# Performance work log

Hardware: AMD Instinct MI355X
Metric: run time of the kernel (lower is better)

Reference implementation:

```python
import jax, jax.numpy as jnp
import numpy as np

HEADS = 12


def setup_inputs() -> dict:
    rng = jax.random.key(0)
    ks = jax.random.split(rng, 12)
    B, L, D = 8, 64, 768
    s = 1.0 / np.sqrt(D)  # keep projections well-scaled
    return {
        "key": jax.random.normal(ks[0], (B, L, L, D), jnp.float32),
        "value": jax.random.normal(ks[1], (B, L, L, D), jnp.float32),
        "query": jax.random.normal(ks[2], (B, L, D), jnp.float32),
        "mask": jnp.ones((B, L, L), jnp.float32),
        "Wk": jax.random.normal(ks[3], (D, D), jnp.float32) * s,
        "bk": jax.random.normal(ks[4], (D,), jnp.float32) * 0.01,
        "Wv": jax.random.normal(ks[5], (D, D), jnp.float32) * s,
        "bv": jax.random.normal(ks[6], (D,), jnp.float32) * 0.01,
        "Wq": jax.random.normal(ks[7], (D, D), jnp.float32) * s,
        "bq": jax.random.normal(ks[8], (D,), jnp.float32) * 0.01,
        "Wo": jax.random.normal(ks[9], (D, D), jnp.float32) * s,
        "bo": jax.random.normal(ks[10], (D,), jnp.float32) * 0.01,
    }


def reference(key, value, query, mask, Wk, bk, Wv, bv, Wq, bq, Wo, bo):
    # key/value: [B, L, L, D]; query: [B, L, D]; mask: [B, L, L]
    B, L, _, D = key.shape
    h = HEADS
    d = D // h
    # Projections (torch Linear y = x W^T + b; here W stored transposed so y = x @ W + b)
    Kp = (key @ Wk + bk).reshape(B, L, L, h, d)    # [B, i, j, h, d]
    Vp = (value @ Wv + bv).reshape(B, L, L, h, d)  # [B, i, j, h, d]
    Qp = (query @ Wq + bq).reshape(B, L, h, d)     # [B, i, h, d]
    Qp = Qp / jnp.sqrt(jnp.asarray(d, Qp.dtype))
    # scores[b,h,i,j] = sum_d Q[b,i,h,d] * K[b,i,j,h,d]  (query i attends over its own j-row)
    scores = jnp.einsum('bihd,bijhd->bhij', Qp, Kp)
    # multiplicative mask (as in the original: scores = scores * mask)
    scores = scores * mask[:, None, :, :]
    attn = jax.nn.softmax(scores, axis=-1)
    # dropout is identity at inference
    ctx = jnp.einsum('bhij,bijhd->bihd', attn, Vp).reshape(B, L, D)
    return ctx @ Wo + bo  # [B, L, D]
```

## Files before the change

### kernel.cpp

```cpp
#include <hip/hip_runtime.h>

#define DMODEL 768
#define NHEADS 12
#define RTOT   512
#define BIW    9216

__global__ __launch_bounds__(256) void linear16(
    const float* __restrict__ src, int ars, int scm,
    const float* __restrict__ W, const float* __restrict__ bias,
    float* __restrict__ dst, int drs, float scale)
{
    __shared__ float At[16][64];
    __shared__ float Bt[64][32];
    const int rt = blockIdx.x, ct = blockIdx.y, t = threadIdx.x;
    const int sk = ((ct * 32) >> 6) * scm;
    const int c  = t & 31;
    const int rg = t >> 5;

    const int ar0 = t >> 4,          ak0 = t & 15;
    const int bk0 = t >> 3,          bc0 = (t & 7) * 4;
    const int bk1 = (t + 256) >> 3,  bc1 = ((t + 256) & 7) * 4;

    float4 va0, vb0, vb1;
    auto LD = [&](int kb) {
        va0 = *(const float4*)&src[(size_t)(rt * 16 + ar0) * ars + sk + kb * 64 + ak0 * 4];
        vb0 = *(const float4*)&W[(size_t)(kb * 64 + bk0) * DMODEL + ct * 32 + bc0];
        vb1 = *(const float4*)&W[(size_t)(kb * 64 + bk1) * DMODEL + ct * 32 + bc1];
    };

    LD(0);
    float acc[2] = {0.f, 0.f};

    for (int kb = 0; kb < 12; ++kb) {
        if (kb) __syncthreads();
        *(float4*)&At[ar0][ak0 * 4] = va0;
        *(float4*)&Bt[bk0][bc0] = vb0;
        *(float4*)&Bt[bk1][bc1] = vb1;
        __syncthreads();
        if (kb < 11) LD(kb + 1);
        #pragma unroll
        for (int kq = 0; kq < 16; ++kq) {
            float b0 = Bt[kq * 4 + 0][c], b1 = Bt[kq * 4 + 1][c];
            float b2 = Bt[kq * 4 + 2][c], b3 = Bt[kq * 4 + 3][c];
            #pragma unroll
            for (int i = 0; i < 2; ++i) {
                float4 a = *(const float4*)&At[rg * 2 + i][kq * 4];
                acc[i] += a.x * b0 + a.y * b1 + a.z * b2 + a.w * b3;
            }
        }
    }
    const float bb = bias[ct * 32 + c];
    #pragma unroll
    for (int i = 0; i < 2; ++i)
        dst[(size_t)(rt * 16 + rg * 2 + i) * drs + ct * 32 + c] = (acc[i] + bb) * scale;
}

__global__ __launch_bounds__(256) void u_kernel(
    const float* __restrict__ qp, const float* __restrict__ Wk, const float* __restrict__ bk,
    float* __restrict__ u, float* __restrict__ cvec)
{
    __shared__ float Qt[32][64];
    __shared__ float Bt[64][65];
    const int rt = blockIdx.x, mt = blockIdx.y, h = blockIdx.z, t = threadIdx.x;

    #pragma unroll
    for (int kk = 0; kk < 2; ++kk) {
        int i4 = t + kk * 256;
        int r = i4 >> 4, dq = i4 & 15;
        *(float4*)&Qt[r][dq * 4] =
            *(const float4*)&qp[(size_t)(rt * 32 + r) * DMODEL + h * 64 + dq * 4];
    }
    #pragma unroll
    for (int kk = 0; kk < 4; ++kk) {
        int i4 = t + kk * 256;
        int m = i4 >> 4, dq = i4 & 15;
        float4 v = *(const float4*)&Wk[(size_t)(mt * 64 + m) * DMODEL + h * 64 + dq * 4];
        Bt[m][dq * 4 + 0] = v.x; Bt[m][dq * 4 + 1] = v.y;
        Bt[m][dq * 4 + 2] = v.z; Bt[m][dq * 4 + 3] = v.w;
    }
    __syncthreads();

    const int c = t & 63, rg = t >> 6;
    float acc[8] = {0.f,0.f,0.f,0.f,0.f,0.f,0.f,0.f};
    #pragma unroll
    for (int dq = 0; dq < 16; ++dq) {
        float b0 = Bt[c][dq * 4 + 0], b1 = Bt[c][dq * 4 + 1];
        float b2 = Bt[c][dq * 4 + 2], b3 = Bt[c][dq * 4 + 3];
        #pragma unroll
        for (int i = 0; i < 8; ++i) {
            float4 a = *(const float4*)&Qt[rg * 8 + i][dq * 4];
            acc[i] += a.x * b0 + a.y * b1 + a.z * b2 + a.w * b3;
        }
    }
    #pragma unroll
    for (int i = 0; i < 8; ++i)
        u[(size_t)(rt * 32 + rg * 8 + i) * BIW + h * DMODEL + mt * 64 + c] = acc[i];

    if (mt == 0 && t < 32) {
        float s = 0.f;
        for (int d = 0; d < 64; ++d) s += bk[h * 64 + d] * Qt[t][d];
        cvec[(rt * 32 + t) * NHEADS + h] = s;
    }
}

__global__ __launch_bounds__(256) void scores_k(
    const float* __restrict__ key, const float* __restrict__ u,
    const float* __restrict__ cvec, const float* __restrict__ mask,
    float* __restrict__ sc_out)
{
    const int bi   = blockIdx.x;
    const int jh   = blockIdx.y;
    const int t    = threadIdx.x;
    const int lane = t & 63;
    const int wv   = t >> 6;
    const size_t kvb = (size_t)bi * 64 * DMODEL;
    const float* ub = u + (size_t)bi * BIW + lane * 4;

    #pragma unroll
    for (int pass = 0; pass < 4; ++pass) {
        const int j0 = jh * 32 + wv * 8 + pass * 2;
        float a[NHEADS][2];
        #pragma unroll
        for (int h = 0; h < NHEADS; ++h) { a[h][0] = 0.f; a[h][1] = 0.f; }

        const float* k0 = &key[kvb + (size_t)j0 * DMODEL + lane * 4];
        float4 kc[2], kn[2];
        kc[0] = *(const float4*)k0;
        kc[1] = *(const float4*)(k0 + DMODEL);

        #pragma unroll
        for (int cch = 0; cch < 3; ++cch) {
            if (cch < 2) {
                kn[0] = *(const float4*)(k0 + (cch + 1) * 256);
                kn[1] = *(const float4*)(k0 + DMODEL + (cch + 1) * 256);
            }
            #pragma unroll
            for (int h = 0; h < NHEADS; ++h) {
                float4 u4 = *(const float4*)(ub + h * DMODEL + cch * 256);
                a[h][0] += kc[0].x * u4.x + kc[0].y * u4.y + kc[0].z * u4.z + kc[0].w * u4.w;
                a[h][1] += kc[1].x * u4.x + kc[1].y * u4.y + kc[1].z * u4.z + kc[1].w * u4.w;
            }
            kc[0] = kn[0];
            kc[1] = kn[1];
        }

        #pragma unroll
        for (int r = 0; r < 2; ++r) {
            float s6[6];
            #pragma unroll
            for (int i = 0; i < 6; ++i) {
                float lo = a[i][r], hi = a[i + 6][r];
                float tl = __shfl_xor(lo, 32), th = __shfl_xor(hi, 32);
                s6[i] = (lane < 32) ? lo + tl : hi + th;
            }
            float s3[3];
            #pragma unroll
            for (int i = 0; i < 3; ++i) {
                float lo = s6[i], hi = s6[i + 3];
                float tl = __shfl_xor(lo, 16), th = __shfl_xor(hi, 16);
                s3[i] = ((lane & 16) == 0) ? lo + tl : hi + th;
            }
            #pragma unroll
            for (int o = 8; o >= 1; o >>= 1)
                #pragma unroll
                for (int i = 0; i < 3; ++i) s3[i] += __shfl_xor(s3[i], o);
            if ((lane & 15) == 0) {
                const int g = lane >> 4;
                const int j = j0 + r;
                const float mk = mask[bi * 64 + j];
                #pragma unroll
                for (int i = 0; i < 3; ++i) {
                    const int h = g * 3 + i;
                    sc_out[(size_t)bi * 768 + h * 64 + j] =
                        (s3[i] + cvec[bi * NHEADS + h]) * mk;
                }
            }
        }
    }
}

__global__ __launch_bounds__(256) void pv_k(
    const float* __restrict__ value, const float* __restrict__ sc,
    float* __restrict__ w)
{
    __shared__ float attn[NHEADS][64];

    const int bi   = blockIdx.x;
    const int ms   = blockIdx.y;
    const int t    = threadIdx.x;
    const int lane = t & 63;
    const int wv   = t >> 6;
    const size_t kvb = (size_t)bi * 64 * DMODEL;

    #pragma unroll
    for (int i = 0; i < 3; ++i) {
        const int h = wv * 3 + i;
        float s = sc[(size_t)bi * 768 + h * 64 + lane];
        float mx = s;
        #pragma unroll
        for (int o = 1; o < 64; o <<= 1) mx = fmaxf(mx, __shfl_xor(mx, o));
        float e = __expf(s - mx);
        float sm = e;
        #pragma unroll
        for (int o = 1; o < 64; o <<= 1) sm += __shfl_xor(sm, o);
        attn[h][lane] = e / sm;
    }
    __syncthreads();

    const int mo = ms * 256 + t;
    float acc[NHEADS];
    #pragma unroll
    for (int h = 0; h < NHEADS; ++h) acc[h] = 0.f;
    const float* vb = value + kvb + mo;

    #pragma unroll 2
    for (int j4 = 0; j4 < 64; j4 += 4) {
        float v0 = vb[(size_t)(j4 + 0) * DMODEL];
        float v1 = vb[(size_t)(j4 + 1) * DMODEL];
        float v2 = vb[(size_t)(j4 + 2) * DMODEL];
        float v3 = vb[(size_t)(j4 + 3) * DMODEL];
        #pragma unroll
        for (int h = 0; h < NHEADS; ++h) {
            float4 at = *(const float4*)&attn[h][j4];
            acc[h] += at.x * v0 + at.y * v1 + at.z * v2 + at.w * v3;
        }
    }
    #pragma unroll
    for (int h = 0; h < NHEADS; ++h)
        w[(size_t)bi * BIW + h * DMODEL + mo] = acc[h];
}

extern "C" void kernel_launch(void* const* d_in, const int* in_sizes, int n_in,
                              void* d_out, int out_size, void* d_ws, size_t ws_size,
                              hipStream_t stream) {
    const float* key   = (const float*)d_in[0];
    const float* value = (const float*)d_in[1];
    const float* query = (const float*)d_in[2];
    const float* mask  = (const float*)d_in[3];
    const float* Wk    = (const float*)d_in[4];
    const float* bk    = (const float*)d_in[5];
    const float* Wv    = (const float*)d_in[6];
    const float* bv    = (const float*)d_in[7];
    const float* Wq    = (const float*)d_in[8];
    const float* bq    = (const float*)d_in[9];
    const float* Wo    = (const float*)d_in[10];
    const float* bo    = (const float*)d_in[11];
    float* out = (float*)d_out;

    float* wsf    = (float*)d_ws;
    float* qp_ctx = wsf;
    float* u_w    = wsf + (size_t)RTOT * DMODEL;
    float* cvec   = u_w + (size_t)RTOT * BIW;
    float* sc_ws  = cvec + (size_t)RTOT * NHEADS;

    linear16<<<dim3(32, 24), 256, 0, stream>>>(query, DMODEL, 0, Wq, bq, qp_ctx, DMODEL, 0.125f);
    u_kernel<<<dim3(16, 12, 12), 256, 0, stream>>>(qp_ctx, Wk, bk, u_w, cvec);
    scores_k<<<dim3(512, 2), 256, 0, stream>>>(key, u_w, cvec, mask, sc_ws);
    pv_k<<<dim3(512, 3), 256, 0, stream>>>(value, sc_ws, u_w);
    linear16<<<dim3(32, 24), 256, 0, stream>>>(u_w, BIW, DMODEL, Wv, bv, qp_ctx, DMODEL, 1.0f);
    linear16<<<dim3(32, 24), 256, 0, stream>>>(qp_ctx, DMODEL, 0, Wo, bo, out, DMODEL, 1.0f);
}
```

Baseline: 177.2 us.

## Split heads across waves in scores kernel and keep u slices in registers

The scores kernel used to give each wave its own rows of j and loop over all 12 heads, reloading u from memory for every row pair. Now each wave owns 3 heads, holds their u vectors in registers for the whole block, and works through 4 key rows per iteration with a shorter shuffle reduction. As a result every wave of the block reads the same key rows, so key traffic is served from cache rather than each wave streaming separate rows. Launch bounds now request 4 blocks per CU, which limits registers, and the k4 and uf register arrays could spill.

```diff
diff --git a/kernel.cpp b/kernel.cpp
--- a/kernel.cpp
+++ b/kernel.cpp
@@ -103,7 +103,7 @@
     }
 }
 
-__global__ __launch_bounds__(256) void scores_k(
+__global__ __launch_bounds__(256, 4) void scores_k(
     const float* __restrict__ key, const float* __restrict__ u,
     const float* __restrict__ cvec, const float* __restrict__ mask,
     float* __restrict__ sc_out)
@@ -113,68 +113,77 @@
     const int t    = threadIdx.x;
     const int lane = t & 63;
     const int wv   = t >> 6;
+    const int h0   = wv * 3;
     const size_t kvb = (size_t)bi * 64 * DMODEL;
-    const float* ub = u + (size_t)bi * BIW + lane * 4;
-
-    #pragma unroll
-    for (int pass = 0; pass < 4; ++pass) {
-        const int j0 = jh * 32 + wv * 8 + pass * 2;
-        float a[NHEADS][2];
-        #pragma unroll
-        for (int h = 0; h < NHEADS; ++h) { a[h][0] = 0.f; a[h][1] = 0.f; }
-
-        const float* k0 = &key[kvb + (size_t)j0 * DMODEL + lane * 4];
-        float4 kc[2], kn[2];
-        kc[0] = *(const float4*)k0;
-        kc[1] = *(const float4*)(k0 + DMODEL);
-
-        #pragma unroll
-        for (int cch = 0; cch < 3; ++cch) {
-            if (cch < 2) {
-                kn[0] = *(const float4*)(k0 + (cch + 1) * 256);
-                kn[1] = *(const float4*)(k0 + DMODEL + (cch + 1) * 256);
+
+    float4 uf[3][3];
+    #pragma unroll
+    for (int i = 0; i < 3; ++i)
+        #pragma unroll
+        for (int cch = 0; cch < 3; ++cch)
+            uf[i][cch] = *(const float4*)&u[(size_t)bi * BIW + (h0 + i) * DMODEL + cch * 256 + lane * 4];
+
+    const float cv0 = cvec[bi * NHEADS + h0 + 0];
+    const float cv1 = cvec[bi * NHEADS + h0 + 1];
+    const float cv2 = cvec[bi * NHEADS + h0 + 2];
+
+    #pragma unroll 1
+    for (int b = 0; b < 8; ++b) {
+        const int j0 = jh * 32 + b * 4;
+        const float* kp = &key[kvb + (size_t)j0 * DMODEL + lane * 4];
+
+        float4 k4[4][3];
+        #pragma unroll
+        for (int r = 0; r < 4; ++r)
+            #pragma unroll
+            for (int cch = 0; cch < 3; ++cch)
+                k4[r][cch] = *(const float4*)(kp + (size_t)r * DMODEL + cch * 256);
+
+        float v[3][4];
+        #pragma unroll
+        for (int i = 0; i < 3; ++i)
+            #pragma unroll
+            for (int r = 0; r < 4; ++r) v[i][r] = 0.f;
+
+        #pragma unroll
+        for (int cch = 0; cch < 3; ++cch)
+            #pragma unroll
+            for (int i = 0; i < 3; ++i) {
+                const float4 uu = uf[i][cch];
+                #pragma unroll
+                for (int r = 0; r < 4; ++r)
+                    v[i][r] += k4[r][cch].x * uu.x + k4[r][cch].y * uu.y
+                             + k4[r][cch].z * uu.z + k4[r][cch].w * uu.w;
             }
-            #pragma unroll
-            for (int h = 0; h < NHEADS; ++h) {
-                float4 u4 = *(const float4*)(ub + h * DMODEL + cch * 256);
-                a[h][0] += kc[0].x * u4.x + kc[0].y * u4.y + kc[0].z * u4.z + kc[0].w * u4.w;
-                a[h][1] += kc[1].x * u4.x + kc[1].y * u4.y + kc[1].z * u4.z + kc[1].w * u4.w;
+
+        float s[3][2];
+        #pragma unroll
+        for (int i = 0; i < 3; ++i)
+            #pragma unroll
+            for (int r = 0; r < 2; ++r) {
+                float lo = v[i][r], hi = v[i][r + 2];
+                float tl = __shfl_xor(lo, 32), th = __shfl_xor(hi, 32);
+                s[i][r] = (lane < 32) ? lo + tl : hi + th;
             }
-            kc[0] = kn[0];
-            kc[1] = kn[1];
-        }
-
-        #pragma unroll
-        for (int r = 0; r < 2; ++r) {
-            float s6[6];
-            #pragma unroll
-            for (int i = 0; i < 6; ++i) {
-                float lo = a[i][r], hi = a[i + 6][r];
-                float tl = __shfl_xor(lo, 32), th = __shfl_xor(hi, 32);
-                s6[i] = (lane < 32) ? lo + tl : hi + th;
-            }
-            float s3[3];
-            #pragma unroll
-            for (int i = 0; i < 3; ++i) {
-                float lo = s6[i], hi = s6[i + 3];
-                float tl = __shfl_xor(lo, 16), th = __shfl_xor(hi, 16);
-                s3[i] = ((lane & 16) == 0) ? lo + tl : hi + th;
-            }
-            #pragma unroll
-            for (int o = 8; o >= 1; o >>= 1)
-                #pragma unroll
-                for (int i = 0; i < 3; ++i) s3[i] += __shfl_xor(s3[i], o);
-            if ((lane & 15) == 0) {
-                const int g = lane >> 4;
-                const int j = j0 + r;
-                const float mk = mask[bi * 64 + j];
-                #pragma unroll
-                for (int i = 0; i < 3; ++i) {
-                    const int h = g * 3 + i;
-                    sc_out[(size_t)bi * 768 + h * 64 + j] =
-                        (s3[i] + cvec[bi * NHEADS + h]) * mk;
-                }
-            }
+        float tt[3];
+        #pragma unroll
+        for (int i = 0; i < 3; ++i) {
+            float lo = s[i][0], hi = s[i][1];
+            float tl = __shfl_xor(lo, 16), th = __shfl_xor(hi, 16);
+            tt[i] = ((lane & 16) == 0) ? lo + tl : hi + th;
+        }
+        #pragma unroll
+        for (int o = 8; o >= 1; o >>= 1)
+            #pragma unroll
+            for (int i = 0; i < 3; ++i) tt[i] += __shfl_xor(tt[i], o);
+
+        if ((lane & 15) == 0) {
+            const int q = lane >> 4;
+            const int j = j0 + q;
+            const float mk = mask[bi * 64 + j];
+            sc_out[(size_t)bi * 768 + (h0 + 0) * 64 + j] = (tt[0] + cv0) * mk;
+            sc_out[(size_t)bi * 768 + (h0 + 1) * 64 + j] = (tt[1] + cv1) * mk;
+            sc_out[(size_t)bi * 768 + (h0 + 2) * 64 + j] = (tt[2] + cv2) * mk;
         }
     }
 }
```

New measurement: 161.2 us. 9.0% less time.
